# Optimization experiments

Hardware: AMD Instinct MI355X
Metric: run time of the kernel (lower is better)

The kernel has to match this reference:

```python
import jax, jax.numpy as jnp
import numpy as np

B, T, Z, X, R, HT, HO = 512, 256, 128, 64, 1024, 1024, 1024


def _linear(x, w, b):
    return x @ w.T + b


def _loc_scale(x, p):
    # p = (gate_ih_w, gate_ih_b, gate_hz_w, gate_hz_b,
    #      prop_ih_w, prop_ih_b, prop_hz_w, prop_hz_b,
    #      loc_w, loc_b, scale_w, scale_b)
    (g_ih_w, g_ih_b, g_hz_w, g_hz_b,
     p_ih_w, p_ih_b, p_hz_w, p_hz_b,
     l_w, l_b, s_w, s_b) = p
    gate = jax.nn.sigmoid(_linear(jax.nn.relu(_linear(x, g_ih_w, g_ih_b)), g_hz_w, g_hz_b))
    proposed = _linear(jax.nn.relu(_linear(x, p_ih_w, p_ih_b)), p_hz_w, p_hz_b)
    loc = (1.0 - gate) * _linear(x, l_w, l_b) + gate * proposed
    scale = jax.nn.softplus(_linear(jax.nn.relu(proposed), s_w, s_b))
    return loc, scale


def _gru_cell(x, h, w_ih, b_ih, w_hh, b_hh):
    # torch GRUCell: gates ordered (r, z, n)
    gi = x @ w_ih.T + b_ih
    gh = h @ w_hh.T + b_hh
    i_r, i_z, i_n = jnp.split(gi, 3, axis=-1)
    h_r, h_z, h_n = jnp.split(gh, 3, axis=-1)
    r = jax.nn.sigmoid(i_r + h_r)
    z = jax.nn.sigmoid(i_z + h_z)
    n = jnp.tanh(i_n + r * h_n)
    return (1.0 - z) * n + z * h


def _mk_linear(key, out_dim, in_dim, std=0.02):
    kw, kb = jax.random.split(key)
    w = jax.random.normal(kw, (out_dim, in_dim), jnp.float32) * std
    b = jnp.zeros((out_dim,), jnp.float32)
    return w, b


def setup_inputs() -> dict:
    key = jax.random.key(0)
    ks = jax.random.split(key, 20)
    inp = {}
    inp['mini_batch'] = jax.random.normal(ks[0], (B, T, X), jnp.float32)
    inp['eps'] = jax.random.normal(ks[1], (B, T, Z), jnp.float32)
    inp['z_0'] = jnp.zeros((Z,), jnp.float32)
    inp['h_0'] = jnp.zeros((R,), jnp.float32)
    # GRUCell params
    inp['gru_w_ih'], inp['gru_b_ih'] = _mk_linear(ks[2], 3 * R, Z)
    inp['gru_w_hh'], inp['gru_b_hh'] = _mk_linear(ks[3], 3 * R, R)
    # trans LocScaleTransformer: in=R, out=Z, hidden=HT
    inp['t_gate_ih_w'], inp['t_gate_ih_b'] = _mk_linear(ks[4], HT, R)
    inp['t_gate_hz_w'], inp['t_gate_hz_b'] = _mk_linear(ks[5], Z, HT)
    inp['t_prop_ih_w'], inp['t_prop_ih_b'] = _mk_linear(ks[6], HT, R)
    inp['t_prop_hz_w'], inp['t_prop_hz_b'] = _mk_linear(ks[7], Z, HT)
    inp['t_loc_w'], inp['t_loc_b'] = _mk_linear(ks[8], Z, R)
    inp['t_scale_w'], inp['t_scale_b'] = _mk_linear(ks[9], Z, Z)
    # obs LocScaleTransformer: in=Z, out=X, hidden=HO
    inp['o_gate_ih_w'], inp['o_gate_ih_b'] = _mk_linear(ks[10], HO, Z)
    inp['o_gate_hz_w'], inp['o_gate_hz_b'] = _mk_linear(ks[11], X, HO)
    inp['o_prop_ih_w'], inp['o_prop_ih_b'] = _mk_linear(ks[12], HO, Z)
    inp['o_prop_hz_w'], inp['o_prop_hz_b'] = _mk_linear(ks[13], X, HO)
    inp['o_loc_w'], inp['o_loc_b'] = _mk_linear(ks[14], X, Z)
    inp['o_scale_w'], inp['o_scale_b'] = _mk_linear(ks[15], X, X)
    return inp


def reference(mini_batch, eps, z_0, h_0,
              gru_w_ih, gru_b_ih, gru_w_hh, gru_b_hh,
              t_gate_ih_w, t_gate_ih_b, t_gate_hz_w, t_gate_hz_b,
              t_prop_ih_w, t_prop_ih_b, t_prop_hz_w, t_prop_hz_b,
              t_loc_w, t_loc_b, t_scale_w, t_scale_b,
              o_gate_ih_w, o_gate_ih_b, o_gate_hz_w, o_gate_hz_b,
              o_prop_ih_w, o_prop_ih_b, o_prop_hz_w, o_prop_hz_b,
              o_loc_w, o_loc_b, o_scale_w, o_scale_b):
    b = mini_batch.shape[0]
    trans_p = (t_gate_ih_w, t_gate_ih_b, t_gate_hz_w, t_gate_hz_b,
               t_prop_ih_w, t_prop_ih_b, t_prop_hz_w, t_prop_hz_b,
               t_loc_w, t_loc_b, t_scale_w, t_scale_b)
    obs_p = (o_gate_ih_w, o_gate_ih_b, o_gate_hz_w, o_gate_hz_b,
             o_prop_ih_w, o_prop_ih_b, o_prop_hz_w, o_prop_hz_b,
             o_loc_w, o_loc_b, o_scale_w, o_scale_b)

    z_prev = jnp.broadcast_to(z_0, (b, z_0.shape[0]))
    h_prev = jnp.broadcast_to(h_0, (b, h_0.shape[0]))

    def step(carry, eps_t):
        z_p, h_p = carry
        rnn_out = _gru_cell(z_p, h_p, gru_w_ih, gru_b_ih, gru_w_hh, gru_b_hh)
        z_loc, z_scale = _loc_scale(rnn_out, trans_p)
        z_t = z_loc + z_scale * eps_t  # reparameterized Normal sample
        x_loc, x_scale = _loc_scale(z_t, obs_p)
        return (z_t, rnn_out), jnp.concatenate([x_loc, x_scale], axis=-1)

    # scan over time: eps -> [T, B, Z]
    _, out = jax.lax.scan(step, (z_prev, h_prev), eps.transpose(1, 0, 2))
    return out.transpose(1, 0, 2)  # [B, T, 2*X]
```

## Files before the change

kernel.cpp:

```cpp
#include <hip/hip_runtime.h>
#include <math.h>


typedef unsigned short u16;
typedef unsigned long long u64;
typedef __bf16 bf16x8 __attribute__((ext_vector_type(8)));
typedef u16    u16x8  __attribute__((ext_vector_type(8)));
typedef float  f32x4  __attribute__((ext_vector_type(4)));

#define DI __device__ __forceinline__
#define LDS_STRIDE 72

DI u16  f2b(float f){ union{float f; unsigned u;} c; c.f = f;
                      return (u16)((c.u + 0x7fffu + ((c.u>>16)&1u))>>16); }
DI float b2f(u16 x){ union{unsigned u; float f;} c; c.u = ((unsigned)x)<<16; return c.f; }
DI float sigm (float x){ return 1.f/(1.f+expf(-x)); }
DI float softp(float x){ return (x>15.f)? x : log1pf(expf(x)); }

DI f32x4 mfma16(bf16x8 a, bf16x8 b, f32x4 c){
  return __builtin_amdgcn_mfma_f32_16x16x32_bf16(a,b,c,0,0,0);
}
DI bf16x8 ldw8b(const u16* __restrict__ g){
  return __builtin_bit_cast(bf16x8, *(const u16x8*)g);
}
DI bf16x8 ldfragS(const u16* l, int row, int ko, int stride){
  return __builtin_bit_cast(bf16x8, *(const u16x8*)(l + row*stride + ko));
}
DI bf16x8 ldfrag(const u16* l, int row, int ko){ return ldfragS(l, row, ko, LDS_STRIDE); }

DI u64 ldc64(const void* p){
  return __hip_atomic_load((const u64*)p, __ATOMIC_RELAXED, __HIP_MEMORY_SCOPE_AGENT);
}
DI u16 ldc16(const u16* p){
  return __hip_atomic_load(p, __ATOMIC_RELAXED, __HIP_MEMORY_SCOPE_AGENT);
}
DI void stc16(u16* p, u16 v){
  __hip_atomic_store(p, v, __ATOMIC_RELAXED, __HIP_MEMORY_SCOPE_AGENT);
}
DI float ldc32f(const float* p){
  unsigned u = __hip_atomic_load((const unsigned*)p, __ATOMIC_RELAXED, __HIP_MEMORY_SCOPE_AGENT);
  union{unsigned u; float f;} c; c.u = u; return c.f;
}
DI void stc32f(float* p, float v){
  union{float f; unsigned u;} c; c.f = v;
  __hip_atomic_store((unsigned*)p, c.u, __ATOMIC_RELAXED, __HIP_MEMORY_SCOPE_AGENT);
}
DI void stage_cg(const u16* g, u16* l){
  u64 a = ldc64(g), b = ldc64(g + 4);
  *(u64*)l = a; *(u64*)(l + 4) = b;
}

DI void gsync(unsigned* bar, unsigned bi, int blk){
  __syncthreads();
  if(threadIdx.x == 0){
    unsigned v = __hip_atomic_fetch_add(bar + (blk & 7)*32, 1u,
                   __ATOMIC_RELAXED, __HIP_MEMORY_SCOPE_AGENT);
    if(v == bi*64u + 63u){
      unsigned r = __hip_atomic_fetch_add(bar + 256, 1u,
                     __ATOMIC_RELAXED, __HIP_MEMORY_SCOPE_AGENT);
      if(r == bi*8u + 7u)
        __hip_atomic_store(bar + 288, bi + 1u,
                           __ATOMIC_RELAXED, __HIP_MEMORY_SCOPE_AGENT);
    }
    while(__hip_atomic_load(bar + 288, __ATOMIC_RELAXED,
                            __HIP_MEMORY_SCOPE_AGENT) <= bi)
      __builtin_amdgcn_s_sleep(4);
  }
  asm volatile("" ::: "memory");
  __syncthreads();
}

__global__ __launch_bounds__(256) void k_cvt(const float* __restrict__ s,
                                             u16* __restrict__ d){
  int i = (blockIdx.x*256 + threadIdx.x)*8;
  f32x4 p0 = *(const f32x4*)(s+i), p1 = *(const f32x4*)(s+i+4);
  u16x8 o;
  o[0]=f2b(p0[0]); o[1]=f2b(p0[1]); o[2]=f2b(p0[2]); o[3]=f2b(p0[3]);
  o[4]=f2b(p1[0]); o[5]=f2b(p1[1]); o[6]=f2b(p1[2]); o[7]=f2b(p1[3]);
  *(u16x8*)(d+i) = o;
}

__global__ __launch_bounds__(256) void k_init(u16* __restrict__ hb,
                                              u16* __restrict__ zb,
                                              const float* __restrict__ h0,
                                              const float* __restrict__ z0){
  int idx = blockIdx.x*256 + threadIdx.x;
  hb[idx] = f2b(h0[idx & 1023]);
  if(idx < 512*128) zb[idx] = f2b(z0[idx & 127]);
}

__global__ void k_bzero(unsigned* b){ b[threadIdx.x] = 0u; b[threadIdx.x+256] = 0u; }

struct SeqP {
  const float *eps, *h0, *z0;
  const float *gbih, *gbhh, *tgb, *tpb, *tlb, *tghzb, *tphzb, *tsb;
  const u16 *wih, *whh, *tgw, *tpw, *tlw, *tghzw, *tphzw, *tsw;
  float *out, *GP;
  u16 *Hbuf, *hb16, *zb16;
  unsigned *bar;
};

DI void mlp_tile(const u16* __restrict__ A,
                 const u16* __restrict__ W,
                 const float* __restrict__ bias, int act,
                 u16* __restrict__ Cb,
                 u16* smem, int tid)
{
  const int lane=tid&63, w=tid>>6, l16=lane&15, quad=lane>>4, wm=w>>1, wn=w&1;
  const int ar=tid>>3, ac=(tid&7)*8, br=tid>>2, bc=(tid&3)*16;
  f32x4 acc[2] = {};
#pragma unroll 1
  for(int it=-1; it<16; ++it){
    int is = it+1;
    if(is < 16){
      u16* b = smem + (is&1)*6912;
      stage_cg(A + (size_t)ar*1024 + is*64 + ac, b + ar*LDS_STRIDE + ac);
      u16* lb = b + 2304;
      *(u16x8*)(lb + br*LDS_STRIDE + bc) =
        *(const u16x8*)(W + (size_t)br*1024 + is*64 + bc);
      *(u16x8*)(lb + br*LDS_STRIDE + bc + 8) =
        *(const u16x8*)(W + (size_t)br*1024 + is*64 + bc + 8);
    }
    if(it >= 0){
      u16* c = smem + (it&1)*6912;
#pragma unroll
      for(int kc=0;kc<2;kc++){
        int ko = kc*32 + quad*8;
        bf16x8 a  = ldfrag(c, wm*16 + l16, ko);
        bf16x8 b0 = ldfrag(c + 2304, wn*32 + l16, ko);
        bf16x8 b1 = ldfrag(c + 2304, wn*32 + 16 + l16, ko);
        acc[0] = mfma16(a, b0, acc[0]);
        acc[1] = mfma16(a, b1, acc[1]);
      }
    }
    __syncthreads();
  }
#pragma unroll
  for(int nf=0; nf<2; nf++)
#pragma unroll
  for(int i=0; i<4; i++){
    int m  = wm*16 + quad*4 + i;
    int cl = wn*32 + nf*16 + l16;
    float v = acc[nf][i] + bias[cl];
    if(act) v = fmaxf(v, 0.f);
    stc16(&Cb[(size_t)m*2176 + cl], f2b(v));
  }
}

__global__ __launch_bounds__(256, 2) void k_seq(SeqP p)
{
  __shared__ u16 smem[18432];
  const int blk  = blockIdx.x;
  const int tid  = threadIdx.x;
  const int lane = tid & 63, w = tid >> 6;
  const int l16  = lane & 15, quad = lane >> 4;
  const int wm   = w >> 1, wn = w & 1;
  const int ar   = tid >> 3, ac = (tid & 7) * 8;

  const int p1m0 = (blk >> 5) * 32;
  const int p1n0 = (blk & 31) * 32;
  const int p1n  = p1n0 + wn*16 + l16;
  f32x4 hreg;
  { float h0v = p.h0[p1n]; hreg[0]=h0v; hreg[1]=h0v; hreg[2]=h0v; hreg[3]=h0v; }

  unsigned bi = 0;

#pragma unroll 1
  for(int t = 0; t < 256; t++){
    const u16* hbi = p.hb16 + (size_t)(t&1)*524288;
    u16*       hbo = p.hb16 + (size_t)((t+1)&1)*524288;

    {
      f32x4 acc[4] = {};
#pragma unroll 1
      for(int it=-1; it<18; ++it){
        int is = it+1;
        if(is < 18){
          u16* b = smem + (is&1)*9216;
          const u16* A; const u16* W; int ld, k0;
          if(is < 2){ A = p.zb16 + (size_t)p1m0*128;  W = p.wih; ld = 128;  k0 = is*64; }
          else      { A = hbi    + (size_t)p1m0*1024; W = p.whh; ld = 1024; k0 = (is-2)*64; }
          stage_cg(A + (size_t)ar*ld + k0 + ac, b + ar*LDS_STRIDE + ac);
#pragma unroll
          for(int s=0; s<3; s++)
            *(u16x8*)(b + 2304 + s*2304 + ar*LDS_STRIDE + ac) =
              *(const u16x8*)(W + (size_t)(s*1024 + p1n0 + ar)*ld + k0 + ac);
        }
        if(it >= 0){
          u16* c = smem + (it&1)*9216;
          int ai3 = (it < 2) ? 2 : 3;
#pragma unroll
          for(int kc=0; kc<2; kc++){
            int ko = kc*32 + quad*8;
            bf16x8 a = ldfrag(c, wm*16 + l16, ko);
#pragma unroll
            for(int s=0; s<3; s++){
              int ai = (s==2) ? ai3 : s;
              bf16x8 bb = ldfrag(c + 2304 + s*2304, wn*16 + l16, ko);
              acc[ai] = mfma16(a, bb, acc[ai]);
            }
          }
        }
        __syncthreads();
      }
#pragma unroll
      for(int i=0; i<4; i++){
        int m = p1m0 + wm*16 + quad*4 + i;
        int n = p1n;
        float r  = sigm (acc[0][i] + p.gbih[n]      + p.gbhh[n]);
        float z  = sigm (acc[1][i] + p.gbih[n+1024] + p.gbhh[n+1024]);
        float nn = tanhf(acc[2][i] + p.gbih[n+2048]
                         + r*(acc[3][i] + p.gbhh[n+2048]));
        float hv = (1.f-z)*nn + z*hreg[i];
        hreg[i] = hv;
        stc16(&hbo[(size_t)m*1024 + n], f2b(hv));
      }
    }
    gsync(p.bar, bi++, blk);

    {
      const int m0 = (blk >> 5) * 32;
      const int n0 = (blk & 31) * 64;
      const u16* W; const float* bias;
      if(n0 < 1024){ W = p.tgw + (size_t)n0*1024;        bias = p.tgb + n0; }
      else         { W = p.tpw + (size_t)(n0-1024)*1024; bias = p.tpb + (n0-1024); }
      mlp_tile(hbo + (size_t)m0*1024, W, bias, 1,
               p.Hbuf + (size_t)m0*2176 + n0, smem, tid);
    }
    gsync(p.bar, bi++, blk);

    if(blk < 128){
      const int m0 = (blk >> 3) * 32, n0 = (blk & 7) * 32;
      const int reg1 = (n0 >= 128);
      const u16*  A = p.Hbuf + (size_t)m0*2176 + (reg1 ? 1024 : 0);
      const u16*  W = reg1 ? p.tphzw + (size_t)(n0-128)*1024
                           : p.tghzw + (size_t)n0*1024;
      const float* bias = reg1 ? p.tphzb + (n0-128) : p.tghzb + n0;
      f32x4 acc3 = {};
#pragma unroll 1
      for(int it=-1; it<16; ++it){
        int is = it+1;
        if(is < 16){
          u16* b = smem + (is&1)*4608;
          stage_cg(A + (size_t)ar*2176 + is*64 + ac, b + ar*LDS_STRIDE + ac);
          *(u16x8*)(b + 2304 + ar*LDS_STRIDE + ac) =
            *(const u16x8*)(W + (size_t)ar*1024 + is*64 + ac);
        }
        if(it >= 0){
          u16* c = smem + (it&1)*4608;
#pragma unroll
          for(int kc=0; kc<2; kc++){
            int ko = kc*32 + quad*8;
            acc3 = mfma16(ldfrag(c, wm*16 + l16, ko),
                          ldfrag(c + 2304, wn*16 + l16, ko), acc3);
          }
        }
        __syncthreads();
      }
#pragma unroll
      for(int i=0; i<4; i++){
        int m  = m0 + wm*16 + quad*4 + i;
        int cl = wn*16 + l16;
        stc32f(&p.GP[(size_t)m*256 + n0 + cl], acc3[i] + bias[cl]);
      }
    } else if(blk < 160){
      const int idx = blk - 128;
      const int m0  = (idx & 15) * 32;
      const int n0l = 2048 + (idx >> 4) * 64;
      mlp_tile(hbo + (size_t)m0*1024, p.tlw + (size_t)(n0l-2048)*1024,
               p.tlb + (n0l-2048), 0,
               p.Hbuf + (size_t)m0*2176 + n0l, smem, tid);
    }
    gsync(p.bar, bi++, blk);

    if(blk < 64){
      const int m0 = (blk >> 1) * 16, n0 = (blk & 1) * 64;
      u16* lp = smem;
      {
        int r = tid >> 4, c = (tid & 15) * 8;
        const float* src = p.GP + (size_t)(m0+r)*256 + 128 + c;
        union{u64 q; float f[2];} q0,q1,q2,q3;
        q0.q = ldc64(src);   q1.q = ldc64(src+2);
        q2.q = ldc64(src+4); q3.q = ldc64(src+6);
        u16x8 o;
        o[0]=f2b(fmaxf(q0.f[0],0.f)); o[1]=f2b(fmaxf(q0.f[1],0.f));
        o[2]=f2b(fmaxf(q1.f[0],0.f)); o[3]=f2b(fmaxf(q1.f[1],0.f));
        o[4]=f2b(fmaxf(q2.f[0],0.f)); o[5]=f2b(fmaxf(q2.f[1],0.f));
        o[6]=f2b(fmaxf(q3.f[0],0.f)); o[7]=f2b(fmaxf(q3.f[1],0.f));
        *(u16x8*)(lp + r*136 + c) = o;
      }
      __syncthreads();
      f32x4 acc4 = {};
      const int col = n0 + w*16 + l16;
#pragma unroll
      for(int kc=0; kc<4; kc++){
        int ko = kc*32 + quad*8;
        acc4 = mfma16(ldfragS(lp, l16, ko, 136),
                      ldw8b(p.tsw + (size_t)col*128 + ko), acc4);
      }
#pragma unroll
      for(int i=0; i<4; i++){
        int gm = m0 + quad*4 + i;
        float zs  = softp(acc4[i] + p.tsb[col]);
        float g   = sigm(ldc32f(&p.GP[(size_t)gm*256 + col]));
        float pv  = ldc32f(&p.GP[(size_t)gm*256 + 128 + col]);
        float loc = b2f(ldc16(&p.Hbuf[(size_t)gm*2176 + 2048 + col]));
        float zl  = (1.f-g)*loc + g*pv;
        float e   = p.eps[(size_t)gm*32768 + (size_t)t*128 + col];
        float zv  = zl + zs*e;
        p.out[(size_t)gm*32768 + (size_t)t*128 + col] = zv;
        stc16(&p.zb16[(size_t)gm*128 + col], f2b(zv));
      }
    }
    gsync(p.bar, bi++, blk);
  }
}

#define LH_S 520
__global__ __launch_bounds__(256) void k_obs(
  const u16* __restrict__ ogw,   const float* __restrict__ ogb,
  const u16* __restrict__ oghzw, const float* __restrict__ oghzb,
  const u16* __restrict__ opw,   const float* __restrict__ opb,
  const u16* __restrict__ ophzw, const float* __restrict__ ophzb,
  const u16* __restrict__ olw,   const float* __restrict__ olb,
  const u16* __restrict__ osw,   const float* __restrict__ osb,
  float* __restrict__ out)
{
  __shared__ u16 lz[32*136];
  __shared__ u16 lh[32*LH_S];
  __shared__ u16 lp[32*72];
  const int r0 = blockIdx.x*32;
  const int t  = r0 >> 9, b0 = r0 & 511;
  const int tid = threadIdx.x;
  const int lane = tid & 63, w = tid>>6, l16 = lane&15, quad = lane>>4;

#pragma unroll
  for(int i=0;i<2;i++){
    int ch = tid + i*256;
    int r = ch>>4, c = (ch&15)*8;
    const float* src = out + (size_t)(b0+r)*32768 + (size_t)t*128 + c;
    f32x4 p0 = *(const f32x4*)src, p1 = *(const f32x4*)(src+4);
    u16x8 o;
    o[0]=f2b(p0[0]); o[1]=f2b(p0[1]); o[2]=f2b(p0[2]); o[3]=f2b(p0[3]);
    o[4]=f2b(p1[0]); o[5]=f2b(p1[1]); o[6]=f2b(p1[2]); o[7]=f2b(p1[3]);
    *(u16x8*)(lz + r*136 + c) = o;
  }
  __syncthreads();

  f32x4 accp[2] = {}, accg[2] = {};
  const int col = w*16 + l16;

#pragma unroll 1
  for(int ph=0; ph<2; ph++){
    const u16* hw = ph ? ogw   : opw;
    const float* hb = ph ? ogb : opb;
    const u16* zw = ph ? oghzw : ophzw;
    f32x4* acc2    = ph ? accg : accp;
#pragma unroll 1
    for(int c2=0; c2<2; c2++){
      __syncthreads();
      for(int nt = w; nt < 32; nt += 4){
        int n = c2*512 + nt*16 + l16;
#pragma unroll
        for(int mi=0; mi<2; mi++){
          f32x4 a = {};
#pragma unroll
          for(int kc=0;kc<4;kc++){
            int ko = kc*32 + quad*8;
            a = mfma16(ldfragS(lz, mi*16+l16, ko, 136),
                       ldw8b(hw + (size_t)n*128 + ko), a);
          }
          float bias = hb[n];
#pragma unroll
          for(int i=0;i<4;i++)
            lh[(mi*16+quad*4+i)*LH_S + nt*16 + l16] = f2b(fmaxf(a[i]+bias, 0.f));
        }
      }
      __syncthreads();
#pragma unroll
      for(int mi=0;mi<2;mi++){
        f32x4 a = acc2[mi];
        for(int kc=0;kc<16;kc++){
          int ko = kc*32 + quad*8;
          a = mfma16(ldfragS(lh, mi*16+l16, ko, LH_S),
                     ldw8b(zw + (size_t)col*1024 + c2*512 + ko), a);
        }
        acc2[mi] = a;
      }
    }
    if(ph==0){
      float bias = ophzb[col];
#pragma unroll
      for(int mi=0;mi<2;mi++)
#pragma unroll
      for(int i=0;i<4;i++){
        float pv = accp[mi][i] + bias;
        accp[mi][i] = pv;
        lp[(mi*16+quad*4+i)*72 + col] = f2b(fmaxf(pv, 0.f));
      }
    }
  }

  f32x4 accl[2]={}, accs[2]={};
#pragma unroll
  for(int mi=0;mi<2;mi++){
#pragma unroll
    for(int kc=0;kc<4;kc++){
      int ko=kc*32+quad*8;
      accl[mi]=mfma16(ldfragS(lz,mi*16+l16,ko,136),
                      ldw8b(olw + (size_t)col*128 + ko), accl[mi]);
    }
#pragma unroll
    for(int kc=0;kc<2;kc++){
      int ko=kc*32+quad*8;
      accs[mi]=mfma16(ldfragS(lp,mi*16+l16,ko,72),
                      ldw8b(osw + (size_t)col*64 + ko), accs[mi]);
    }
  }
#pragma unroll
  for(int mi=0;mi<2;mi++)
#pragma unroll
  for(int i=0;i<4;i++){
    int r = mi*16 + quad*4 + i;
    float g  = sigm(accg[mi][i] + oghzb[col]);
    float pv = accp[mi][i];
    float lc = accl[mi][i] + olb[col];
    float xs = softp(accs[mi][i] + osb[col]);
    float xl = (1.f-g)*lc + g*pv;
    size_t o = (size_t)(b0+r)*32768 + (size_t)t*128 + col;
    out[o]      = xl;
    out[o + 64] = xs;
  }
}

extern "C" void kernel_launch(void* const* d_in, const int* in_sizes, int n_in,
                              void* d_out, int out_size, void* d_ws, size_t ws_size,
                              hipStream_t stream)
{
  (void)in_sizes; (void)n_in; (void)out_size; (void)ws_size;
  const float* eps   = (const float*)d_in[1];
  const float* z0    = (const float*)d_in[2];
  const float* h0    = (const float*)d_in[3];
  const float* gwih  = (const float*)d_in[4];  const float* gbih  = (const float*)d_in[5];
  const float* gwhh  = (const float*)d_in[6];  const float* gbhh  = (const float*)d_in[7];
  const float* tgw   = (const float*)d_in[8];  const float* tgb   = (const float*)d_in[9];
  const float* tghzw = (const float*)d_in[10]; const float* tghzb = (const float*)d_in[11];
  const float* tpw   = (const float*)d_in[12]; const float* tpb   = (const float*)d_in[13];
  const float* tphzw = (const float*)d_in[14]; const float* tphzb = (const float*)d_in[15];
  const float* tlw   = (const float*)d_in[16]; const float* tlb   = (const float*)d_in[17];
  const float* tsw   = (const float*)d_in[18]; const float* tsb   = (const float*)d_in[19];
  const float* ogw   = (const float*)d_in[20]; const float* ogb   = (const float*)d_in[21];
  const float* oghzw = (const float*)d_in[22]; const float* oghzb = (const float*)d_in[23];
  const float* opw   = (const float*)d_in[24]; const float* opb   = (const float*)d_in[25];
  const float* ophzw = (const float*)d_in[26]; const float* ophzb = (const float*)d_in[27];
  const float* olw   = (const float*)d_in[28]; const float* olb   = (const float*)d_in[29];
  const float* osw   = (const float*)d_in[30]; const float* osb   = (const float*)d_in[31];
  float* out = (float*)d_out;

  char* ws = (char*)d_ws;
  size_t off = 0;
  u16*   Hbuf = (u16*)  (ws + off); off += (size_t)512*2176*2;
  float* GP   = (float*)(ws + off); off += (size_t)512*256*4;
  u16*   hb16 = (u16*)  (ws + off); off += (size_t)2*512*1024*2;
  u16*   zb16 = (u16*)  (ws + off); off += (size_t)512*128*2;
  u16* wc_gwih  = (u16*)(ws + off); off += (size_t)3072*128 *2;
  u16* wc_gwhh  = (u16*)(ws + off); off += (size_t)3072*1024*2;
  u16* wc_tgw   = (u16*)(ws + off); off += (size_t)1024*1024*2;
  u16* wc_tpw   = (u16*)(ws + off); off += (size_t)1024*1024*2;
  u16* wc_tlw   = (u16*)(ws + off); off += (size_t)128*1024 *2;
  u16* wc_tghzw = (u16*)(ws + off); off += (size_t)128*1024 *2;
  u16* wc_tphzw = (u16*)(ws + off); off += (size_t)128*1024 *2;
  u16* wc_tsw   = (u16*)(ws + off); off += (size_t)128*128  *2;
  u16* wc_ogw   = (u16*)(ws + off); off += (size_t)1024*128 *2;
  u16* wc_opw   = (u16*)(ws + off); off += (size_t)1024*128 *2;
  u16* wc_oghzw = (u16*)(ws + off); off += (size_t)64*1024  *2;
  u16* wc_ophzw = (u16*)(ws + off); off += (size_t)64*1024  *2;
  u16* wc_olw   = (u16*)(ws + off); off += (size_t)64*128   *2;
  u16* wc_osw   = (u16*)(ws + off); off += (size_t)64*64    *2;
  unsigned* bar = (unsigned*)(ws + off); off += 2048;

  #define CVT(src, dst, n) k_cvt<<<(n)/2048, 256, 0, stream>>>((src), (dst))
  CVT(gwih,  wc_gwih,  3072*128);
  CVT(gwhh,  wc_gwhh,  3072*1024);
  CVT(tgw,   wc_tgw,   1024*1024);
  CVT(tpw,   wc_tpw,   1024*1024);
  CVT(tlw,   wc_tlw,   128*1024);
  CVT(tghzw, wc_tghzw, 128*1024);
  CVT(tphzw, wc_tphzw, 128*1024);
  CVT(tsw,   wc_tsw,   128*128);
  CVT(ogw,   wc_ogw,   1024*128);
  CVT(opw,   wc_opw,   1024*128);
  CVT(oghzw, wc_oghzw, 64*1024);
  CVT(ophzw, wc_ophzw, 64*1024);
  CVT(olw,   wc_olw,   64*128);
  CVT(osw,   wc_osw,   64*64);
  #undef CVT
  k_init <<<2048, 256, 0, stream>>>(hb16, zb16, h0, z0);
  k_bzero<<<1, 256, 0, stream>>>(bar);

  SeqP sp;
  sp.eps = eps; sp.h0 = h0; sp.z0 = z0;
  sp.gbih = gbih; sp.gbhh = gbhh;
  sp.tgb = tgb; sp.tpb = tpb; sp.tlb = tlb;
  sp.tghzb = tghzb; sp.tphzb = tphzb; sp.tsb = tsb;
  sp.wih = wc_gwih; sp.whh = wc_gwhh;
  sp.tgw = wc_tgw; sp.tpw = wc_tpw; sp.tlw = wc_tlw;
  sp.tghzw = wc_tghzw; sp.tphzw = wc_tphzw; sp.tsw = wc_tsw;
  sp.out = out; sp.GP = GP;
  sp.Hbuf = Hbuf; sp.hb16 = hb16; sp.zb16 = zb16;
  sp.bar = bar;
  k_seq<<<512, 256, 0, stream>>>(sp);

  k_obs<<<4096, 256, 0, stream>>>(wc_ogw, ogb, wc_oghzw, oghzb,
                                  wc_opw, opb, wc_ophzw, ophzb,
                                  wc_olw, olb, wc_osw, osb, out);
}
```

Measured before the change: 13.37 ms.

## Prefetch global tiles into registers several K-steps ahead in GEMM loops

Rewrites the three main K-loops (GRU gates, MLP hidden tile, hz projection) so global loads for later K-steps are issued into a register ring several iterations ahead. Each step stores registers to LDS, syncs with a raw barrier, then issues the next loads before the MFMAs. This is meant to hide global and L2 latency inside a latency-bound persistent recurrent kernel. It costs extra registers per thread, which could hurt occupancy under the 2-blocks launch bound.

New measurement: 10.77 ms. -19.5%, faster.

```diff
diff --git a/kernel.cpp b/kernel.cpp
--- a/kernel.cpp
+++ b/kernel.cpp
@@ -31,6 +31,9 @@
 DI u64 ldc64(const void* p){
   return __hip_atomic_load((const u64*)p, __ATOMIC_RELAXED, __HIP_MEMORY_SCOPE_AGENT);
 }
+DI u16x8 ldc128(const u16* g){
+  union{u64 q[2]; u16x8 v;} u; u.q[0] = ldc64(g); u.q[1] = ldc64(g + 4); return u.v;
+}
 DI u16 ldc16(const u16* p){
   return __hip_atomic_load(p, __ATOMIC_RELAXED, __HIP_MEMORY_SCOPE_AGENT);
 }
@@ -44,10 +47,6 @@
 DI void stc32f(float* p, float v){
   union{float f; unsigned u;} c; c.f = v;
   __hip_atomic_store((unsigned*)p, c.u, __ATOMIC_RELAXED, __HIP_MEMORY_SCOPE_AGENT);
-}
-DI void stage_cg(const u16* g, u16* l){
-  u64 a = ldc64(g), b = ldc64(g + 4);
-  *(u64*)l = a; *(u64*)(l + 4) = b;
 }
 
 DI void gsync(unsigned* bar, unsigned bi, int blk){
@@ -109,32 +108,43 @@
   const int lane=tid&63, w=tid>>6, l16=lane&15, quad=lane>>4, wm=w>>1, wn=w&1;
   const int ar=tid>>3, ac=(tid&7)*8, br=tid>>2, bc=(tid&3)*16;
   f32x4 acc[2] = {};
+  u16x8 a0,a1,a2,a3,u0,u1,u2,u3,v0,v1,v2,v3;
+#define MT_ISSUE(ra,ru,rv,is) do{ \
+    ra = ldc128(A + (size_t)ar*1024 + (is)*64 + ac); \
+    ru = *(const u16x8*)(W + (size_t)br*1024 + (is)*64 + bc); \
+    rv = *(const u16x8*)(W + (size_t)br*1024 + (is)*64 + bc + 8); \
+  }while(0)
+#define MT_STEP(ra,ru,rv,it,nx) do{ \
+    u16* b_ = smem + ((it)&1)*6912; \
+    *(u16x8*)(b_ + ar*LDS_STRIDE + ac) = ra; \
+    *(u16x8*)(b_ + 2304 + br*LDS_STRIDE + bc) = ru; \
+    *(u16x8*)(b_ + 2304 + br*LDS_STRIDE + bc + 8) = rv; \
+    asm volatile("s_waitcnt lgkmcnt(0)" ::: "memory"); \
+    __builtin_amdgcn_s_barrier(); \
+    __builtin_amdgcn_sched_barrier(0); \
+    if((nx) < 16) MT_ISSUE(ra,ru,rv,(nx)); \
+    _Pragma("unroll") \
+    for(int kc=0;kc<2;kc++){ \
+      int ko = kc*32 + quad*8; \
+      bf16x8 aa = ldfrag(b_, wm*16 + l16, ko); \
+      bf16x8 q0 = ldfrag(b_ + 2304, wn*32 + l16, ko); \
+      bf16x8 q1 = ldfrag(b_ + 2304, wn*32 + 16 + l16, ko); \
+      acc[0] = mfma16(aa,q0,acc[0]); \
+      acc[1] = mfma16(aa,q1,acc[1]); \
+    } \
+  }while(0)
+  MT_ISSUE(a0,u0,v0,0); MT_ISSUE(a1,u1,v1,1);
+  MT_ISSUE(a2,u2,v2,2); MT_ISSUE(a3,u3,v3,3);
 #pragma unroll 1
-  for(int it=-1; it<16; ++it){
-    int is = it+1;
-    if(is < 16){
-      u16* b = smem + (is&1)*6912;
-      stage_cg(A + (size_t)ar*1024 + is*64 + ac, b + ar*LDS_STRIDE + ac);
-      u16* lb = b + 2304;
-      *(u16x8*)(lb + br*LDS_STRIDE + bc) =
-        *(const u16x8*)(W + (size_t)br*1024 + is*64 + bc);
-      *(u16x8*)(lb + br*LDS_STRIDE + bc + 8) =
-        *(const u16x8*)(W + (size_t)br*1024 + is*64 + bc + 8);
-    }
-    if(it >= 0){
-      u16* c = smem + (it&1)*6912;
-#pragma unroll
-      for(int kc=0;kc<2;kc++){
-        int ko = kc*32 + quad*8;
-        bf16x8 a  = ldfrag(c, wm*16 + l16, ko);
-        bf16x8 b0 = ldfrag(c + 2304, wn*32 + l16, ko);
-        bf16x8 b1 = ldfrag(c + 2304, wn*32 + 16 + l16, ko);
-        acc[0] = mfma16(a, b0, acc[0]);
-        acc[1] = mfma16(a, b1, acc[1]);
-      }
-    }
-    __syncthreads();
-  }
+  for(int ib=0; ib<16; ib+=4){
+    MT_STEP(a0,u0,v0, ib+0, ib+4);
+    MT_STEP(a1,u1,v1, ib+1, ib+5);
+    MT_STEP(a2,u2,v2, ib+2, ib+6);
+    MT_STEP(a3,u3,v3, ib+3, ib+7);
+  }
+#undef MT_ISSUE
+#undef MT_STEP
+  __syncthreads();
 #pragma unroll
   for(int nf=0; nf<2; nf++)
 #pragma unroll
@@ -172,37 +182,51 @@
 
     {
       f32x4 acc[4] = {};
+      u16x8 a0,a1,a2, w00,w01,w02, w10,w11,w12, w20,w21,w22;
+#define P1_ISSUE(ra,r0,r1,r2,is) do{ \
+      const u16 *A_, *W_; int ld_, k0_; \
+      if((is) < 2){ A_ = p.zb16 + (size_t)p1m0*128;  W_ = p.wih; ld_=128;  k0_=(is)*64; } \
+      else        { A_ = hbi    + (size_t)p1m0*1024; W_ = p.whh; ld_=1024; k0_=((is)-2)*64; } \
+      ra = ldc128(A_ + (size_t)ar*ld_ + k0_ + ac); \
+      r0 = *(const u16x8*)(W_ + (size_t)(p1n0 + ar)*ld_        + k0_ + ac); \
+      r1 = *(const u16x8*)(W_ + (size_t)(1024 + p1n0 + ar)*ld_ + k0_ + ac); \
+      r2 = *(const u16x8*)(W_ + (size_t)(2048 + p1n0 + ar)*ld_ + k0_ + ac); \
+    }while(0)
+#define P1_STEP(ra,r0,r1,r2,it,nx) do{ \
+      u16* b_ = smem + ((it)&1)*9216; \
+      *(u16x8*)(b_ + ar*LDS_STRIDE + ac) = ra; \
+      *(u16x8*)(b_ + 2304 + ar*LDS_STRIDE + ac) = r0; \
+      *(u16x8*)(b_ + 4608 + ar*LDS_STRIDE + ac) = r1; \
+      *(u16x8*)(b_ + 6912 + ar*LDS_STRIDE + ac) = r2; \
+      asm volatile("s_waitcnt lgkmcnt(0)" ::: "memory"); \
+      __builtin_amdgcn_s_barrier(); \
+      __builtin_amdgcn_sched_barrier(0); \
+      if((nx) < 18) P1_ISSUE(ra,r0,r1,r2,(nx)); \
+      const int ai3_ = ((it) < 2) ? 2 : 3; \
+      _Pragma("unroll") \
+      for(int kc=0;kc<2;kc++){ \
+        int ko = kc*32 + quad*8; \
+        bf16x8 aa  = ldfrag(b_, wm*16 + l16, ko); \
+        bf16x8 b0v = ldfrag(b_ + 2304, wn*16 + l16, ko); \
+        bf16x8 b1v = ldfrag(b_ + 4608, wn*16 + l16, ko); \
+        bf16x8 b2v = ldfrag(b_ + 6912, wn*16 + l16, ko); \
+        acc[0]    = mfma16(aa,b0v,acc[0]); \
+        acc[1]    = mfma16(aa,b1v,acc[1]); \
+        acc[ai3_] = mfma16(aa,b2v,acc[ai3_]); \
+      } \
+    }while(0)
+      P1_ISSUE(a0,w00,w01,w02,0);
+      P1_ISSUE(a1,w10,w11,w12,1);
+      P1_ISSUE(a2,w20,w21,w22,2);
 #pragma unroll 1
-      for(int it=-1; it<18; ++it){
-        int is = it+1;
-        if(is < 18){
-          u16* b = smem + (is&1)*9216;
-          const u16* A; const u16* W; int ld, k0;
-          if(is < 2){ A = p.zb16 + (size_t)p1m0*128;  W = p.wih; ld = 128;  k0 = is*64; }
-          else      { A = hbi    + (size_t)p1m0*1024; W = p.whh; ld = 1024; k0 = (is-2)*64; }
-          stage_cg(A + (size_t)ar*ld + k0 + ac, b + ar*LDS_STRIDE + ac);
-#pragma unroll
-          for(int s=0; s<3; s++)
-            *(u16x8*)(b + 2304 + s*2304 + ar*LDS_STRIDE + ac) =
-              *(const u16x8*)(W + (size_t)(s*1024 + p1n0 + ar)*ld + k0 + ac);
-        }
-        if(it >= 0){
-          u16* c = smem + (it&1)*9216;
-          int ai3 = (it < 2) ? 2 : 3;
-#pragma unroll
-          for(int kc=0; kc<2; kc++){
-            int ko = kc*32 + quad*8;
-            bf16x8 a = ldfrag(c, wm*16 + l16, ko);
-#pragma unroll
-            for(int s=0; s<3; s++){
-              int ai = (s==2) ? ai3 : s;
-              bf16x8 bb = ldfrag(c + 2304 + s*2304, wn*16 + l16, ko);
-              acc[ai] = mfma16(a, bb, acc[ai]);
-            }
-          }
-        }
-        __syncthreads();
-      }
+      for(int ib=0; ib<18; ib+=3){
+        P1_STEP(a0,w00,w01,w02, ib+0, ib+3);
+        P1_STEP(a1,w10,w11,w12, ib+1, ib+4);
+        P1_STEP(a2,w20,w21,w22, ib+2, ib+5);
+      }
+#undef P1_ISSUE
+#undef P1_STEP
+      __syncthreads();
 #pragma unroll
       for(int i=0; i<4; i++){
         int m = p1m0 + wm*16 + quad*4 + i;
@@ -237,26 +261,37 @@
                            : p.tghzw + (size_t)n0*1024;
       const float* bias = reg1 ? p.tphzb + (n0-128) : p.tghzb + n0;
       f32x4 acc3 = {};
+      u16x8 a0,a1,a2,a3, q0,q1,q2,q3;
+#define P3_ISSUE(ra,rw,is) do{ \
+      ra = ldc128(A + (size_t)ar*2176 + (is)*64 + ac); \
+      rw = *(const u16x8*)(W + (size_t)ar*1024 + (is)*64 + ac); \
+    }while(0)
+#define P3_STEP(ra,rw,it,nx) do{ \
+      u16* b_ = smem + ((it)&1)*4608; \
+      *(u16x8*)(b_ + ar*LDS_STRIDE + ac) = ra; \
+      *(u16x8*)(b_ + 2304 + ar*LDS_STRIDE + ac) = rw; \
+      asm volatile("s_waitcnt lgkmcnt(0)" ::: "memory"); \
+      __builtin_amdgcn_s_barrier(); \
+      __builtin_amdgcn_sched_barrier(0); \
+      if((nx) < 16) P3_ISSUE(ra,rw,(nx)); \
+      _Pragma("unroll") \
+      for(int kc=0;kc<2;kc++){ \
+        int ko = kc*32 + quad*8; \
+        acc3 = mfma16(ldfrag(b_, wm*16 + l16, ko), \
+                      ldfrag(b_ + 2304, wn*16 + l16, ko), acc3); \
+      } \
+    }while(0)
+      P3_ISSUE(a0,q0,0); P3_ISSUE(a1,q1,1); P3_ISSUE(a2,q2,2); P3_ISSUE(a3,q3,3);
 #pragma unroll 1
-      for(int it=-1; it<16; ++it){
-        int is = it+1;
-        if(is < 16){
-          u16* b = smem + (is&1)*4608;
-          stage_cg(A + (size_t)ar*2176 + is*64 + ac, b + ar*LDS_STRIDE + ac);
-          *(u16x8*)(b + 2304 + ar*LDS_STRIDE + ac) =
-            *(const u16x8*)(W + (size_t)ar*1024 + is*64 + ac);
-        }
-        if(it >= 0){
-          u16* c = smem + (it&1)*4608;
-#pragma unroll
-          for(int kc=0; kc<2; kc++){
-            int ko = kc*32 + quad*8;
-            acc3 = mfma16(ldfrag(c, wm*16 + l16, ko),
-                          ldfrag(c + 2304, wn*16 + l16, ko), acc3);
-          }
-        }
-        __syncthreads();
-      }
+      for(int ib=0; ib<16; ib+=4){
+        P3_STEP(a0,q0, ib+0, ib+4);
+        P3_STEP(a1,q1, ib+1, ib+5);
+        P3_STEP(a2,q2, ib+2, ib+6);
+        P3_STEP(a3,q3, ib+3, ib+7);
+      }
+#undef P3_ISSUE
+#undef P3_STEP
+      __syncthreads();
 #pragma unroll
       for(int i=0; i<4; i++){
         int m  = m0 + wm*16 + quad*4 + i;
```
